# Performance work log

Hardware: AMD Instinct MI355X
Metric: run time of the kernel (lower is better)

## Reference

```python
import jax, jax.numpy as jnp
import numpy as np


def setup_inputs() -> dict:
    key = jax.random.key(0)
    ks = jax.random.split(key, 10)
    B, L, H, E, D = 2, 2048, 16, 64, 64
    d_model = 512
    inp = {
        "queries": jax.random.normal(ks[0], (B, L, H, E), jnp.float32),
        "keys": jax.random.normal(ks[1], (B, L, H, E), jnp.float32),
        "values": jax.random.normal(ks[2], (B, L, H, D), jnp.float32),
        "raw_series": jax.random.normal(ks[3], (B, L, d_model), jnp.float32),
        # learned fusion MLP: Linear(d_model, d_model//2) -> ReLU -> Linear(d_model//2, 1)
        "w1": jax.random.normal(ks[4], (d_model, d_model // 2), jnp.float32) / np.sqrt(d_model),
        "b1": jnp.zeros((d_model // 2,), jnp.float32),
        "w2": jax.random.normal(ks[5], (d_model // 2, 1), jnp.float32) / np.sqrt(d_model // 2),
        "b2": jnp.zeros((1,), jnp.float32),
        # per-head trend scaling, init ones
        "alpha_trend": jnp.ones((H,), jnp.float32),
    }
    return inp


MOMENTUM_ALPHA = 1.0
MOMENTUM_K = 1


def reference(queries, keys, values, raw_series, w1, b1, w2, b2, alpha_trend):
    B, L, H, E = queries.shape
    scale = 1.0 / jnp.sqrt(jnp.asarray(E, queries.dtype))

    # ---- soft momentum bias ----
    # learned fusion: MLP over features -> scalar per position, [B, L]
    h = jax.nn.relu(raw_series @ w1 + b1)
    fused = (h @ w2 + b2)[..., 0]                       # [B, L]
    k = max(1, min(MOMENTUM_K, L - 1))
    momentum = fused[:, k:] - fused[:, :-k]              # [B, L-k]
    momentum = jnp.pad(momentum, ((0, 0), (k, 0)))       # left-pad zeros -> [B, L]
    diff = jnp.abs(momentum[:, :, None] - momentum[:, None, :])  # [B, L, L]
    soft_bias = -MOMENTUM_ALPHA * diff                   # [B, L, L]

    # ---- attention ----
    scores = jnp.einsum('blhe,bshe->bhls', queries, keys)  # [B, H, L, L]
    scores = scores + soft_bias[:, None, :, :] * alpha_trend[None, :, None, None]
    causal = jnp.triu(jnp.ones((L, L), bool), k=1)       # True above diagonal
    scores = jnp.where(causal[None, None], -jnp.inf, scores)
    A = jax.nn.softmax(scale * scores, axis=-1)          # [B, H, L, L]
    V = jnp.einsum('bhls,bshd->blhd', A, values)         # [B, L, H, D]
    return V
```

## Files before the change

### kernel.cpp

```cpp
#include <hip/hip_runtime.h>
#include <math.h>

#define B_ 2
#define L_ 2048
#define H_ 16
#define E_ 64
#define D_ 64
#define DM_ 512
#define DH_ 256

typedef __bf16 bf16_t;
typedef bf16_t bf16x8_t __attribute__((ext_vector_type(8)));
typedef float f32x4_t __attribute__((ext_vector_type(4)));

__device__ __forceinline__ unsigned bpack(float hi, float lo) {
    unsigned uh = __float_as_uint(hi) + 0x8000u;
    unsigned ul = __float_as_uint(lo) + 0x8000u;
    return __builtin_amdgcn_perm(uh, ul, 0x07060302u);
}

__device__ __forceinline__ bf16_t to_bf16(float f) {
    union { float f; unsigned u; } x; x.f = f;
    unsigned r = (x.u + 0x7fffu + ((x.u >> 16) & 1u)) >> 16;
    union { unsigned short s; bf16_t b; } y; y.s = (unsigned short)r;
    return y.b;
}

__global__ __launch_bounds__(256) void transpose_w1_kernel(
        const float* __restrict__ w1, bf16_t* __restrict__ w1t) {
    const int n = blockIdx.x;
    const int t = threadIdx.x;
    #pragma unroll
    for (int u = 0; u < 2; ++u) {
        int k = t + u * 256;
        float v = w1[(size_t)k * DH_ + n];
        w1t[(size_t)n * DM_ + k] = to_bf16(v);
    }
}

__global__ __launch_bounds__(512) void mlp_kernel(
        const float* __restrict__ raw, const bf16_t* __restrict__ w1t,
        const float* __restrict__ b1, const float* __restrict__ w2,
        const float* __restrict__ b2, float* __restrict__ fused) {
    __shared__ bf16_t Rs[16][520];
    __shared__ float pk[4][4][16][17];
    __shared__ float part[4][16];
    const int t = threadIdx.x;
    const int m0 = blockIdx.x * 16;
    #pragma unroll
    for (int u = 0; u < 4; ++u) {
        int idx = t + u * 512;
        int row = idx >> 7;
        int k = (idx & 127) << 2;
        f32x4_t v = *(const f32x4_t*)&raw[(size_t)(m0 + row) * DM_ + k];
        uint2 p;
        p.x = bpack(v[1], v[0]);
        p.y = bpack(v[3], v[2]);
        *(uint2*)&Rs[row][k] = p;
    }
    __syncthreads();
    const int wave = t >> 6;
    const int lane = t & 63;
    const int lrow = lane & 15;
    const int lgrp = lane >> 4;
    const int nq   = wave & 3;
    const int kh   = wave >> 2;
    const int n0w  = nq * 64;
    const int k0   = kh * 256;

    f32x4_t acc[4];
    #pragma unroll
    for (int nt = 0; nt < 4; ++nt) acc[nt] = (f32x4_t){0.f, 0.f, 0.f, 0.f};

    const bf16_t* wbase = w1t + (size_t)(n0w + lrow) * DM_ + k0 + lgrp * 8;
    #pragma unroll
    for (int s = 0; s < 8; ++s) {
        bf16x8_t a = *(const bf16x8_t*)&Rs[lrow][k0 + s * 32 + lgrp * 8];
        #pragma unroll
        for (int nt = 0; nt < 4; ++nt) {
            bf16x8_t b = *(const bf16x8_t*)(wbase + nt * 16 * DM_ + s * 32);
            acc[nt] = __builtin_amdgcn_mfma_f32_16x16x32_bf16(a, b, acc[nt], 0, 0, 0);
        }
    }
    if (kh == 1) {
        #pragma unroll
        for (int nt = 0; nt < 4; ++nt)
            #pragma unroll
            for (int r = 0; r < 4; ++r)
                pk[nq][nt][lgrp * 4 + r][lrow] = acc[nt][r];
    }
    __syncthreads();
    if (kh == 0) {
        float rowpart[4] = {0.f, 0.f, 0.f, 0.f};
        #pragma unroll
        for (int nt = 0; nt < 4; ++nt) {
            int n = n0w + nt * 16 + lrow;
            float b1v = b1[n];
            float w2v = w2[n];
            #pragma unroll
            for (int r = 0; r < 4; ++r) {
                float h = acc[nt][r] + pk[nq][nt][lgrp * 4 + r][lrow] + b1v;
                h = h > 0.f ? h : 0.f;
                rowpart[r] += h * w2v;
            }
        }
        #pragma unroll
        for (int r = 0; r < 4; ++r) {
            float v = rowpart[r];
            v += __shfl_xor(v, 1);
            v += __shfl_xor(v, 2);
            v += __shfl_xor(v, 4);
            v += __shfl_xor(v, 8);
            if (lrow == 0) part[nq][lgrp * 4 + r] = v;
        }
    }
    __syncthreads();
    if (t < 16)
        fused[m0 + t] = part[0][t] + part[1][t] + part[2][t] + part[3][t] + b2[0];
}

struct TileRegs { f32x4_t k[4]; float v[16]; float m; };

__global__ __launch_bounds__(256) void attn_kernel(
        const float* __restrict__ Q, const float* __restrict__ K,
        const float* __restrict__ V, const float* __restrict__ fused,
        const float* __restrict__ alpha_trend, float* __restrict__ out,
        bf16_t* __restrict__ pO, float* __restrict__ prs) {
    __shared__ bf16_t Ks[64][72];
    __shared__ bf16_t Vt[64][70];
    __shared__ unsigned short Ps[4][16][68];
    __shared__ float moms[64];

    const int bid  = blockIdx.x;
    const int bh   = bid & 31;
    const int wid  = bid >> 5;
    int qt, sa, sb, chunk;
    bool split;
    if (wid < 32) {
        qt    = 31 - (wid >> 1);
        chunk = wid & 1;
        int half = (qt + 2) >> 1;
        sa = chunk ? half : 0;
        sb = chunk ? qt + 1 : half;
        split = true;
    } else {
        qt = 47 - wid;
        sa = 0; sb = qt + 1; chunk = 0;
        split = false;
    }
    const int h    = bh & 15;
    const int b    = bh >> 4;
    const int q0   = qt << 6;
    const int tid  = threadIdx.x;
    const int wave = tid >> 6;
    const int lane = tid & 63;
    const int lrow = lane & 15;
    const int lgrp = lane >> 4;

    const float c1      = 0.18033688f;
    const float ascale2 = alpha_trend[h] * c1;
    const size_t bl     = (size_t)b * L_;
    const int qw0       = q0 + wave * 16;

    const float* Kb = K + (bl * H_ + h) * E_;
    const float* Vb = V + (bl * H_ + h) * D_;
    const float* fp = fused + bl;

    const int krow = tid >> 4;
    const int ke0  = (tid & 15) << 2;
    const int vd   = tid & 63;
    const int vsb  = tid >> 6;

    bf16x8_t a_lo, a_hi;
    {
        const float* qp = Q + ((bl + qw0 + lrow) * H_ + h) * E_ + lgrp * 8;
        f32x4_t v0 = *(const f32x4_t*)(qp);
        f32x4_t v1 = *(const f32x4_t*)(qp + 4);
        f32x4_t v2 = *(const f32x4_t*)(qp + 32);
        f32x4_t v3 = *(const f32x4_t*)(qp + 36);
        #pragma unroll
        for (int k = 0; k < 4; ++k) {
            a_lo[k]     = to_bf16(v0[k] * c1);
            a_lo[4 + k] = to_bf16(v1[k] * c1);
            a_hi[k]     = to_bf16(v2[k] * c1);
            a_hi[4 + k] = to_bf16(v3[k] * c1);
        }
    }
    float mq[4];
    #pragma unroll
    for (int r = 0; r < 4; ++r) {
        int l = qw0 + lgrp * 4 + r;
        mq[r] = (l == 0) ? 0.f : fp[l] - fp[l - 1];
    }

    f32x4_t Oacc[4];
    #pragma unroll
    for (int c = 0; c < 4; ++c) Oacc[c] = (f32x4_t){0.f, 0.f, 0.f, 0.f};
    float rowsum[4] = {0.f, 0.f, 0.f, 0.f};

    TileRegs tr;
    #define LOAD_TILE(st_) do {                                                   \
        const int s0_ = (st_) << 6;                                               \
        _Pragma("unroll")                                                         \
        for (int u = 0; u < 4; ++u)                                               \
            tr.k[u] = *(const f32x4_t*)&Kb[(s0_ + krow + u * 16) * (H_ * E_) + ke0]; \
        _Pragma("unroll")                                                         \
        for (int j = 0; j < 16; ++j)                                              \
            tr.v[j] = Vb[(s0_ + vsb * 16 + j) * (H_ * D_) + vd];                  \
        if (tid < 64) {                                                           \
            int l_ = s0_ + tid;                                                   \
            tr.m = (l_ == 0) ? 0.f : fp[l_] - fp[l_ - 1];                         \
        }                                                                         \
    } while (0)

    LOAD_TILE(sa);

    for (int st = sa; st < sb; ++st) {
        __syncthreads();
        #pragma unroll
        for (int u = 0; u < 4; ++u) {
            uint2 p;
            p.x = bpack(tr.k[u][1], tr.k[u][0]);
            p.y = bpack(tr.k[u][3], tr.k[u][2]);
            *(uint2*)&Ks[krow + u * 16][ke0] = p;
        }
        #pragma unroll
        for (int u = 0; u < 4; ++u) {
            unsigned* vp = (unsigned*)&Vt[vd][vsb * 16 + u * 4];
            vp[0] = bpack(tr.v[u * 4 + 1], tr.v[u * 4 + 0]);
            vp[1] = bpack(tr.v[u * 4 + 3], tr.v[u * 4 + 2]);
        }
        if (tid < 64) moms[tid] = tr.m;
        __syncthreads();

        if (st + 1 < sb) LOAD_TILE(st + 1);

        f32x4_t Sacc[4];
        #pragma unroll
        for (int c = 0; c < 4; ++c) Sacc[c] = (f32x4_t){0.f, 0.f, 0.f, 0.f};
        #pragma unroll
        for (int c = 0; c < 4; ++c) {
            bf16x8_t b_lo = *(const bf16x8_t*)&Ks[c * 16 + lrow][lgrp * 8];
            bf16x8_t b_hi = *(const bf16x8_t*)&Ks[c * 16 + lrow][32 + lgrp * 8];
            Sacc[c] = __builtin_amdgcn_mfma_f32_16x16x32_bf16(a_lo, b_lo, Sacc[c], 0, 0, 0);
            Sacc[c] = __builtin_amdgcn_mfma_f32_16x16x32_bf16(a_hi, b_hi, Sacc[c], 0, 0, 0);
        }

        float rowe[4][4];
        #pragma unroll
        for (int c = 0; c < 4; ++c) {
            float ms = moms[c * 16 + lrow];
            #pragma unroll
            for (int r = 0; r < 4; ++r) {
                float arg = Sacc[c][r] - ascale2 * fabsf(mq[r] - ms);
                rowe[c][r] = __builtin_amdgcn_exp2f(arg);
            }
        }
        if (st == qt) {
            const int s0 = st << 6;
            #pragma unroll
            for (int c = 0; c < 4; ++c) {
                int sg = s0 + c * 16 + lrow;
                #pragma unroll
                for (int r = 0; r < 4; ++r)
                    if (sg > qw0 + lgrp * 4 + r) rowe[c][r] = 0.f;
            }
        }
        unsigned short* Psw = &Ps[wave][0][0];
        #pragma unroll
        for (int c = 0; c < 4; ++c) {
            #pragma unroll
            for (int r = 0; r < 4; ++r) {
                Psw[(lgrp * 4 + r) * 68 + c * 16 + lrow] =
                    (unsigned short)(__float_as_uint(rowe[c][r]) >> 16);
                rowsum[r] += rowe[c][r];
            }
        }

        #pragma unroll
        for (int hh = 0; hh < 2; ++hh) {
            union { uint2 u2[2]; bf16x8_t v; } ab;
            ab.u2[0] = *(const uint2*)&Psw[lrow * 68 + hh * 32 + lgrp * 8];
            ab.u2[1] = *(const uint2*)&Psw[lrow * 68 + hh * 32 + lgrp * 8 + 4];
            #pragma unroll
            for (int c2 = 0; c2 < 4; ++c2) {
                union { unsigned u[4]; bf16x8_t v; } bb;
                const unsigned* vp = (const unsigned*)&Vt[c2 * 16 + lrow][hh * 32 + lgrp * 8];
                bb.u[0] = vp[0]; bb.u[1] = vp[1]; bb.u[2] = vp[2]; bb.u[3] = vp[3];
                Oacc[c2] = __builtin_amdgcn_mfma_f32_16x16x32_bf16(ab.v, bb.v, Oacc[c2], 0, 0, 0);
            }
        }
    }

    if (!split) {
        #pragma unroll
        for (int r = 0; r < 4; ++r) {
            float rs = rowsum[r];
            rs += __shfl_xor(rs, 1);
            rs += __shfl_xor(rs, 2);
            rs += __shfl_xor(rs, 4);
            rs += __shfl_xor(rs, 8);
            float inv = 1.f / rs;
            size_t orow = ((bl + qw0 + lgrp * 4 + r) * H_ + h) * D_;
            #pragma unroll
            for (int c = 0; c < 4; ++c)
                out[orow + c * 16 + lrow] = Oacc[c][r] * inv;
        }
    } else {
        const int slot = (bh * 16 + (qt - 16)) * 2 + chunk;
        bf16_t* po = pO + (size_t)slot * 4096;
        float*  pr = prs + (size_t)slot * 64;
        #pragma unroll
        for (int r = 0; r < 4; ++r) {
            float rs = rowsum[r];
            rs += __shfl_xor(rs, 1);
            rs += __shfl_xor(rs, 2);
            rs += __shfl_xor(rs, 4);
            rs += __shfl_xor(rs, 8);
            int q = wave * 16 + lgrp * 4 + r;
            if (lrow == 0) pr[q] = rs;
            #pragma unroll
            for (int c = 0; c < 4; ++c)
                po[q * 64 + c * 16 + lrow] = to_bf16(Oacc[c][r]);
        }
    }
    #undef LOAD_TILE
}

__global__ __launch_bounds__(256) void merge_kernel(
        const bf16_t* __restrict__ pO, const float* __restrict__ prs,
        float* __restrict__ out) {
    const int bid = blockIdx.x;
    const int bh  = bid & 31;
    const int qt  = 16 + (bid >> 5);
    const int h   = bh & 15;
    const int b   = bh >> 4;
    const int t   = threadIdx.x;
    const int q   = t >> 2;
    const int d0  = (t & 3) << 4;

    const int slotA = (bh * 16 + (qt - 16)) * 2;
    const bf16_t* poA = pO + (size_t)slotA * 4096 + q * 64 + d0;
    const bf16_t* poB = poA + 4096;
    float rs = prs[slotA * 64 + q] + prs[(slotA + 1) * 64 + q];
    float inv = 1.f / rs;

    float* op = out + (((size_t)b * L_ + (qt << 6) + q) * H_ + h) * D_ + d0;
    #pragma unroll
    for (int i = 0; i < 16; i += 4) {
        f32x4_t o;
        #pragma unroll
        for (int k = 0; k < 4; ++k)
            o[k] = ((float)poA[i + k] + (float)poB[i + k]) * inv;
        *(f32x4_t*)&op[i] = o;
    }
}

extern "C" void kernel_launch(void* const* d_in, const int* in_sizes, int n_in,
                              void* d_out, int out_size, void* d_ws, size_t ws_size,
                              hipStream_t stream) {
    const float* Q     = (const float*)d_in[0];
    const float* K     = (const float*)d_in[1];
    const float* V     = (const float*)d_in[2];
    const float* raw   = (const float*)d_in[3];
    const float* w1    = (const float*)d_in[4];
    const float* b1    = (const float*)d_in[5];
    const float* w2    = (const float*)d_in[6];
    const float* b2    = (const float*)d_in[7];
    const float* alpha = (const float*)d_in[8];
    float* out = (float*)d_out;

    float* fused = (float*)d_ws;
    bf16_t* w1t  = (bf16_t*)(fused + B_ * L_);
    bf16_t* pO   = w1t + (size_t)DH_ * DM_;
    float* prs   = (float*)(pO + (size_t)1024 * 4096);

    transpose_w1_kernel<<<DH_, 256, 0, stream>>>(w1, w1t);
    mlp_kernel<<<B_ * L_ / 16, 512, 0, stream>>>(raw, w1t, b1, w2, b2, fused);
    attn_kernel<<<1536, 256, 0, stream>>>(Q, K, V, fused, alpha, out, pO, prs);
    merge_kernel<<<512, 256, 0, stream>>>(pO, prs, out);
}
```

Measured before the change: 174.3 us.

## Restructure attention waves to 32 rows and split MLP across blocks

The attention kernel moves to 128-thread blocks where each wave handles two 16-row query tiles. Each K and V fragment read from LDS then feeds two MFMAs, and the register prefetch of the next tile is dropped in favour of direct loads inside the loop. The MLP kernel is split into two blocks per row group that combine partial sums with atomicAdd into a memset-zeroed buffer. The b2 bias is dropped because only differences of fused are used, so it cancels. The w1 transpose now goes through a shared-memory tile with packed bf16 stores. Removing the prefetch exposes global load latency in the attention loop, which the higher occupancy is meant to hide.

```diff
diff --git a/kernel.cpp b/kernel.cpp
--- a/kernel.cpp
+++ b/kernel.cpp
@@ -28,30 +28,45 @@
 
 __global__ __launch_bounds__(256) void transpose_w1_kernel(
         const float* __restrict__ w1, bf16_t* __restrict__ w1t) {
-    const int n = blockIdx.x;
-    const int t = threadIdx.x;
-    #pragma unroll
-    for (int u = 0; u < 2; ++u) {
-        int k = t + u * 256;
-        float v = w1[(size_t)k * DH_ + n];
-        w1t[(size_t)n * DM_ + k] = to_bf16(v);
-    }
-}
-
-__global__ __launch_bounds__(512) void mlp_kernel(
+    __shared__ float sT[64][65];
+    const int t  = threadIdx.x;
+    const int k0 = (blockIdx.x >> 2) * 64;
+    const int n0 = (blockIdx.x & 3) * 64;
+    const int nn = t & 63;
+    #pragma unroll
+    for (int u = 0; u < 16; ++u) {
+        int k = (t >> 6) + u * 4;
+        sT[k][nn] = w1[(size_t)(k0 + k) * DH_ + n0 + nn];
+    }
+    __syncthreads();
+    const int nr = t >> 2;
+    const int kc = (t & 3) * 16;
+    unsigned pk0[8];
+    #pragma unroll
+    for (int j = 0; j < 8; ++j)
+        pk0[j] = bpack(sT[kc + 2 * j + 1][nr], sT[kc + 2 * j][nr]);
+    bf16_t* dst = w1t + (size_t)(n0 + nr) * DM_ + k0 + kc;
+    ((uint2*)dst)[0] = make_uint2(pk0[0], pk0[1]);
+    ((uint2*)dst)[1] = make_uint2(pk0[2], pk0[3]);
+    ((uint2*)dst)[2] = make_uint2(pk0[4], pk0[5]);
+    ((uint2*)dst)[3] = make_uint2(pk0[6], pk0[7]);
+}
+
+__global__ __launch_bounds__(256) void mlp_kernel(
         const float* __restrict__ raw, const bf16_t* __restrict__ w1t,
         const float* __restrict__ b1, const float* __restrict__ w2,
-        const float* __restrict__ b2, float* __restrict__ fused) {
+        float* __restrict__ fused) {
     __shared__ bf16_t Rs[16][520];
-    __shared__ float pk[4][4][16][17];
-    __shared__ float part[4][16];
-    const int t = threadIdx.x;
-    const int m0 = blockIdx.x * 16;
-    #pragma unroll
-    for (int u = 0; u < 4; ++u) {
-        int idx = t + u * 512;
+    __shared__ float pk[2][4][16][17];
+    __shared__ float part[2][16];
+    const int t  = threadIdx.x;
+    const int m0 = (blockIdx.x >> 1) * 16;
+    const int nh = blockIdx.x & 1;
+    #pragma unroll
+    for (int u = 0; u < 8; ++u) {
+        int idx = t + u * 256;
         int row = idx >> 7;
-        int k = (idx & 127) << 2;
+        int k   = (idx & 127) << 2;
         f32x4_t v = *(const f32x4_t*)&raw[(size_t)(m0 + row) * DM_ + k];
         uint2 p;
         p.x = bpack(v[1], v[0]);
@@ -63,9 +78,9 @@
     const int lane = t & 63;
     const int lrow = lane & 15;
     const int lgrp = lane >> 4;
-    const int nq   = wave & 3;
-    const int kh   = wave >> 2;
-    const int n0w  = nq * 64;
+    const int kh   = wave >> 1;
+    const int nq   = wave & 1;
+    const int n0w  = nh * 128 + nq * 64;
     const int k0   = kh * 256;
 
     f32x4_t acc[4];
@@ -99,9 +114,9 @@
             float w2v = w2[n];
             #pragma unroll
             for (int r = 0; r < 4; ++r) {
-                float h = acc[nt][r] + pk[nq][nt][lgrp * 4 + r][lrow] + b1v;
-                h = h > 0.f ? h : 0.f;
-                rowpart[r] += h * w2v;
+                float hv = acc[nt][r] + pk[nq][nt][lgrp * 4 + r][lrow] + b1v;
+                hv = hv > 0.f ? hv : 0.f;
+                rowpart[r] += hv * w2v;
             }
         }
         #pragma unroll
@@ -116,19 +131,17 @@
     }
     __syncthreads();
     if (t < 16)
-        fused[m0 + t] = part[0][t] + part[1][t] + part[2][t] + part[3][t] + b2[0];
-}
-
-struct TileRegs { f32x4_t k[4]; float v[16]; float m; };
-
-__global__ __launch_bounds__(256) void attn_kernel(
+        atomicAdd(&fused[m0 + t], part[0][t] + part[1][t]);
+}
+
+__global__ __launch_bounds__(128, 3) void attn_kernel(
         const float* __restrict__ Q, const float* __restrict__ K,
         const float* __restrict__ V, const float* __restrict__ fused,
         const float* __restrict__ alpha_trend, float* __restrict__ out,
         bf16_t* __restrict__ pO, float* __restrict__ prs) {
     __shared__ bf16_t Ks[64][72];
-    __shared__ bf16_t Vt[64][70];
-    __shared__ unsigned short Ps[4][16][68];
+    __shared__ bf16_t Vt[64][76];
+    __shared__ unsigned short Ps[2][32][68];
     __shared__ float moms[64];
 
     const int bid  = blockIdx.x;
@@ -160,7 +173,7 @@
     const float c1      = 0.18033688f;
     const float ascale2 = alpha_trend[h] * c1;
     const size_t bl     = (size_t)b * L_;
-    const int qw0       = q0 + wave * 16;
+    const int qw0       = q0 + wave * 32;
 
     const float* Kb = K + (bl * H_ + h) * E_;
     const float* Vb = V + (bl * H_ + h) * D_;
@@ -171,160 +184,149 @@
     const int vd   = tid & 63;
     const int vsb  = tid >> 6;
 
-    bf16x8_t a_lo, a_hi;
-    {
-        const float* qp = Q + ((bl + qw0 + lrow) * H_ + h) * E_ + lgrp * 8;
+    bf16x8_t aq[2][2];
+    #pragma unroll
+    for (int mh = 0; mh < 2; ++mh) {
+        const float* qp = Q + ((bl + qw0 + mh * 16 + lrow) * H_ + h) * E_ + lgrp * 8;
         f32x4_t v0 = *(const f32x4_t*)(qp);
         f32x4_t v1 = *(const f32x4_t*)(qp + 4);
         f32x4_t v2 = *(const f32x4_t*)(qp + 32);
         f32x4_t v3 = *(const f32x4_t*)(qp + 36);
         #pragma unroll
         for (int k = 0; k < 4; ++k) {
-            a_lo[k]     = to_bf16(v0[k] * c1);
-            a_lo[4 + k] = to_bf16(v1[k] * c1);
-            a_hi[k]     = to_bf16(v2[k] * c1);
-            a_hi[4 + k] = to_bf16(v3[k] * c1);
-        }
-    }
-    float mq[4];
-    #pragma unroll
-    for (int r = 0; r < 4; ++r) {
-        int l = qw0 + lgrp * 4 + r;
-        mq[r] = (l == 0) ? 0.f : fp[l] - fp[l - 1];
-    }
-
-    f32x4_t Oacc[4];
-    #pragma unroll
-    for (int c = 0; c < 4; ++c) Oacc[c] = (f32x4_t){0.f, 0.f, 0.f, 0.f};
-    float rowsum[4] = {0.f, 0.f, 0.f, 0.f};
-
-    TileRegs tr;
-    #define LOAD_TILE(st_) do {                                                   \
-        const int s0_ = (st_) << 6;                                               \
-        _Pragma("unroll")                                                         \
-        for (int u = 0; u < 4; ++u)                                               \
-            tr.k[u] = *(const f32x4_t*)&Kb[(s0_ + krow + u * 16) * (H_ * E_) + ke0]; \
-        _Pragma("unroll")                                                         \
-        for (int j = 0; j < 16; ++j)                                              \
-            tr.v[j] = Vb[(s0_ + vsb * 16 + j) * (H_ * D_) + vd];                  \
-        if (tid < 64) {                                                           \
-            int l_ = s0_ + tid;                                                   \
-            tr.m = (l_ == 0) ? 0.f : fp[l_] - fp[l_ - 1];                         \
-        }                                                                         \
-    } while (0)
-
-    LOAD_TILE(sa);
+            aq[mh][0][k]     = to_bf16(v0[k] * c1);
+            aq[mh][0][4 + k] = to_bf16(v1[k] * c1);
+            aq[mh][1][k]     = to_bf16(v2[k] * c1);
+            aq[mh][1][4 + k] = to_bf16(v3[k] * c1);
+        }
+    }
+    float mq[2][4];
+    #pragma unroll
+    for (int mh = 0; mh < 2; ++mh)
+        #pragma unroll
+        for (int r = 0; r < 4; ++r) {
+            int l = qw0 + mh * 16 + lgrp * 4 + r;
+            mq[mh][r] = (l == 0) ? 0.f : fp[l] - fp[l - 1];
+        }
+
+    f32x4_t Oacc[2][4];
+    #pragma unroll
+    for (int mh = 0; mh < 2; ++mh)
+        #pragma unroll
+        for (int c = 0; c < 4; ++c) Oacc[mh][c] = (f32x4_t){0.f, 0.f, 0.f, 0.f};
+    float rowsum[2][4] = {{0.f, 0.f, 0.f, 0.f}, {0.f, 0.f, 0.f, 0.f}};
 
     for (int st = sa; st < sb; ++st) {
+        const int s0 = st << 6;
         __syncthreads();
         #pragma unroll
-        for (int u = 0; u < 4; ++u) {
+        for (int u = 0; u < 8; ++u) {
+            int srow = krow + u * 8;
+            f32x4_t kv = *(const f32x4_t*)&Kb[(s0 + srow) * (H_ * E_) + ke0];
             uint2 p;
-            p.x = bpack(tr.k[u][1], tr.k[u][0]);
-            p.y = bpack(tr.k[u][3], tr.k[u][2]);
-            *(uint2*)&Ks[krow + u * 16][ke0] = p;
-        }
-        #pragma unroll
-        for (int u = 0; u < 4; ++u) {
-            unsigned* vp = (unsigned*)&Vt[vd][vsb * 16 + u * 4];
-            vp[0] = bpack(tr.v[u * 4 + 1], tr.v[u * 4 + 0]);
-            vp[1] = bpack(tr.v[u * 4 + 3], tr.v[u * 4 + 2]);
-        }
-        if (tid < 64) moms[tid] = tr.m;
+            p.x = bpack(kv[1], kv[0]);
+            p.y = bpack(kv[3], kv[2]);
+            *(uint2*)&Ks[srow][ke0] = p;
+        }
+        float vv[32];
+        #pragma unroll
+        for (int j = 0; j < 32; ++j)
+            vv[j] = Vb[(s0 + vsb * 32 + j) * (H_ * D_) + vd];
+        #pragma unroll
+        for (int u = 0; u < 8; ++u) {
+            uint2 p;
+            p.x = bpack(vv[u * 4 + 1], vv[u * 4 + 0]);
+            p.y = bpack(vv[u * 4 + 3], vv[u * 4 + 2]);
+            *(uint2*)&Vt[vd][vsb * 32 + u * 4] = p;
+        }
+        if (tid < 64) {
+            int l_ = s0 + tid;
+            moms[tid] = (l_ == 0) ? 0.f : fp[l_] - fp[l_ - 1];
+        }
         __syncthreads();
 
-        if (st + 1 < sb) LOAD_TILE(st + 1);
-
-        f32x4_t Sacc[4];
-        #pragma unroll
-        for (int c = 0; c < 4; ++c) Sacc[c] = (f32x4_t){0.f, 0.f, 0.f, 0.f};
+        f32x4_t Sacc[2][4];
+        #pragma unroll
+        for (int mh = 0; mh < 2; ++mh)
+            #pragma unroll
+            for (int c = 0; c < 4; ++c) Sacc[mh][c] = (f32x4_t){0.f, 0.f, 0.f, 0.f};
         #pragma unroll
         for (int c = 0; c < 4; ++c) {
             bf16x8_t b_lo = *(const bf16x8_t*)&Ks[c * 16 + lrow][lgrp * 8];
             bf16x8_t b_hi = *(const bf16x8_t*)&Ks[c * 16 + lrow][32 + lgrp * 8];
-            Sacc[c] = __builtin_amdgcn_mfma_f32_16x16x32_bf16(a_lo, b_lo, Sacc[c], 0, 0, 0);
-            Sacc[c] = __builtin_amdgcn_mfma_f32_16x16x32_bf16(a_hi, b_hi, Sacc[c], 0, 0, 0);
-        }
-
-        float rowe[4][4];
+            #pragma unroll
+            for (int mh = 0; mh < 2; ++mh) {
+                Sacc[mh][c] = __builtin_amdgcn_mfma_f32_16x16x32_bf16(aq[mh][0], b_lo, Sacc[mh][c], 0, 0, 0);
+                Sacc[mh][c] = __builtin_amdgcn_mfma_f32_16x16x32_bf16(aq[mh][1], b_hi, Sacc[mh][c], 0, 0, 0);
+            }
+        }
+
+        unsigned short* Psw = &Ps[wave][0][0];
         #pragma unroll
         for (int c = 0; c < 4; ++c) {
             float ms = moms[c * 16 + lrow];
-            #pragma unroll
-            for (int r = 0; r < 4; ++r) {
-                float arg = Sacc[c][r] - ascale2 * fabsf(mq[r] - ms);
-                rowe[c][r] = __builtin_amdgcn_exp2f(arg);
-            }
-        }
-        if (st == qt) {
-            const int s0 = st << 6;
-            #pragma unroll
-            for (int c = 0; c < 4; ++c) {
-                int sg = s0 + c * 16 + lrow;
+            int sg = s0 + c * 16 + lrow;
+            #pragma unroll
+            for (int mh = 0; mh < 2; ++mh) {
                 #pragma unroll
-                for (int r = 0; r < 4; ++r)
-                    if (sg > qw0 + lgrp * 4 + r) rowe[c][r] = 0.f;
-            }
-        }
-        unsigned short* Psw = &Ps[wave][0][0];
-        #pragma unroll
-        for (int c = 0; c < 4; ++c) {
-            #pragma unroll
-            for (int r = 0; r < 4; ++r) {
-                Psw[(lgrp * 4 + r) * 68 + c * 16 + lrow] =
-                    (unsigned short)(__float_as_uint(rowe[c][r]) >> 16);
-                rowsum[r] += rowe[c][r];
+                for (int r = 0; r < 4; ++r) {
+                    float arg = Sacc[mh][c][r] - ascale2 * fabsf(mq[mh][r] - ms);
+                    float e = __builtin_amdgcn_exp2f(arg);
+                    if (st == qt && sg > qw0 + mh * 16 + lgrp * 4 + r) e = 0.f;
+                    Psw[(mh * 16 + lgrp * 4 + r) * 68 + c * 16 + lrow] =
+                        (unsigned short)(__float_as_uint(e) >> 16);
+                    rowsum[mh][r] += e;
+                }
             }
         }
 
         #pragma unroll
         for (int hh = 0; hh < 2; ++hh) {
-            union { uint2 u2[2]; bf16x8_t v; } ab;
-            ab.u2[0] = *(const uint2*)&Psw[lrow * 68 + hh * 32 + lgrp * 8];
-            ab.u2[1] = *(const uint2*)&Psw[lrow * 68 + hh * 32 + lgrp * 8 + 4];
+            union { uint2 u2[2]; bf16x8_t v; } ap[2];
+            #pragma unroll
+            for (int mh = 0; mh < 2; ++mh) {
+                ap[mh].u2[0] = *(const uint2*)&Psw[(mh * 16 + lrow) * 68 + hh * 32 + lgrp * 8];
+                ap[mh].u2[1] = *(const uint2*)&Psw[(mh * 16 + lrow) * 68 + hh * 32 + lgrp * 8 + 4];
+            }
             #pragma unroll
             for (int c2 = 0; c2 < 4; ++c2) {
-                union { unsigned u[4]; bf16x8_t v; } bb;
-                const unsigned* vp = (const unsigned*)&Vt[c2 * 16 + lrow][hh * 32 + lgrp * 8];
-                bb.u[0] = vp[0]; bb.u[1] = vp[1]; bb.u[2] = vp[2]; bb.u[3] = vp[3];
-                Oacc[c2] = __builtin_amdgcn_mfma_f32_16x16x32_bf16(ab.v, bb.v, Oacc[c2], 0, 0, 0);
-            }
-        }
-    }
-
-    if (!split) {
+                union { uint2 u2[2]; bf16x8_t v; } bb;
+                bb.u2[0] = *(const uint2*)&Vt[c2 * 16 + lrow][hh * 32 + lgrp * 8];
+                bb.u2[1] = *(const uint2*)&Vt[c2 * 16 + lrow][hh * 32 + lgrp * 8 + 4];
+                #pragma unroll
+                for (int mh = 0; mh < 2; ++mh)
+                    Oacc[mh][c2] = __builtin_amdgcn_mfma_f32_16x16x32_bf16(ap[mh].v, bb.v, Oacc[mh][c2], 0, 0, 0);
+            }
+        }
+    }
+
+    #pragma unroll
+    for (int mh = 0; mh < 2; ++mh) {
         #pragma unroll
         for (int r = 0; r < 4; ++r) {
-            float rs = rowsum[r];
+            float rs = rowsum[mh][r];
             rs += __shfl_xor(rs, 1);
             rs += __shfl_xor(rs, 2);
             rs += __shfl_xor(rs, 4);
             rs += __shfl_xor(rs, 8);
-            float inv = 1.f / rs;
-            size_t orow = ((bl + qw0 + lgrp * 4 + r) * H_ + h) * D_;
-            #pragma unroll
-            for (int c = 0; c < 4; ++c)
-                out[orow + c * 16 + lrow] = Oacc[c][r] * inv;
-        }
-    } else {
-        const int slot = (bh * 16 + (qt - 16)) * 2 + chunk;
-        bf16_t* po = pO + (size_t)slot * 4096;
-        float*  pr = prs + (size_t)slot * 64;
-        #pragma unroll
-        for (int r = 0; r < 4; ++r) {
-            float rs = rowsum[r];
-            rs += __shfl_xor(rs, 1);
-            rs += __shfl_xor(rs, 2);
-            rs += __shfl_xor(rs, 4);
-            rs += __shfl_xor(rs, 8);
-            int q = wave * 16 + lgrp * 4 + r;
-            if (lrow == 0) pr[q] = rs;
-            #pragma unroll
-            for (int c = 0; c < 4; ++c)
-                po[q * 64 + c * 16 + lrow] = to_bf16(Oacc[c][r]);
-        }
-    }
-    #undef LOAD_TILE
+            if (!split) {
+                float inv = 1.f / rs;
+                size_t orow = ((bl + qw0 + mh * 16 + lgrp * 4 + r) * H_ + h) * D_;
+                #pragma unroll
+                for (int c = 0; c < 4; ++c)
+                    out[orow + c * 16 + lrow] = Oacc[mh][c][r] * inv;
+            } else {
+                const int slot = (bh * 16 + (qt - 16)) * 2 + chunk;
+                bf16_t* po = pO + (size_t)slot * 4096;
+                float*  pr = prs + (size_t)slot * 64;
+                int q = wave * 32 + mh * 16 + lgrp * 4 + r;
+                if (lrow == 0) pr[q] = rs;
+                #pragma unroll
+                for (int c = 0; c < 4; ++c)
+                    po[q * 64 + c * 16 + lrow] = to_bf16(Oacc[mh][c][r]);
+            }
+        }
+    }
 }
 
 __global__ __launch_bounds__(256) void merge_kernel(
@@ -366,7 +368,6 @@
     const float* w1    = (const float*)d_in[4];
     const float* b1    = (const float*)d_in[5];
     const float* w2    = (const float*)d_in[6];
-    const float* b2    = (const float*)d_in[7];
     const float* alpha = (const float*)d_in[8];
     float* out = (float*)d_out;
 
@@ -375,8 +376,9 @@
     bf16_t* pO   = w1t + (size_t)DH_ * DM_;
     float* prs   = (float*)(pO + (size_t)1024 * 4096);
 
-    transpose_w1_kernel<<<DH_, 256, 0, stream>>>(w1, w1t);
-    mlp_kernel<<<B_ * L_ / 16, 512, 0, stream>>>(raw, w1t, b1, w2, b2, fused);
-    attn_kernel<<<1536, 256, 0, stream>>>(Q, K, V, fused, alpha, out, pO, prs);
+    hipMemsetAsync(fused, 0, B_ * L_ * sizeof(float), stream);
+    transpose_w1_kernel<<<32, 256, 0, stream>>>(w1, w1t);
+    mlp_kernel<<<B_ * L_ / 16 * 2, 256, 0, stream>>>(raw, w1t, b1, w2, fused);
+    attn_kernel<<<1536, 128, 0, stream>>>(Q, K, V, fused, alpha, out, pO, prs);
     merge_kernel<<<512, 256, 0, stream>>>(pO, prs, out);
 }
```

After: 173.4 us. No clear change (-0.5%).
